# Performance work log

Measured on AMD Instinct MI355X. Metric: run time of the kernel, lower is better.

Reference implementation:

```python
import jax, jax.numpy as jnp
import numpy as np

N, E = 50000, 800000          # nodes, directed edges
IN_DIM, HC, OUT_DIM = 128, 64, 128
NEG_SLOPE = 0.2               # PyG GATConv default leaky_relu slope
EPS = 1e-5                    # PyG LayerNorm default eps


def setup_inputs() -> dict:
    key = jax.random.key(0)
    ks = jax.random.split(key, 10)
    s = 0.1
    return {
        "x": jax.random.normal(ks[0], (N, IN_DIM), jnp.float32),
        "edge_index": jax.random.randint(ks[1], (2, E), 0, N, dtype=jnp.int32),
        # conv1: GATConv(IN_DIM -> HC, heads=2, concat=True)
        "W1": jax.random.normal(ks[2], (IN_DIM, 2 * HC), jnp.float32) * s,
        "att_src1": jax.random.normal(ks[3], (2, HC), jnp.float32) * s,
        "att_dst1": jax.random.normal(ks[4], (2, HC), jnp.float32) * s,
        "b1": jnp.zeros((2 * HC,), jnp.float32),
        "ln1_w": jnp.ones((2 * HC,), jnp.float32),
        "ln1_b": jnp.zeros((2 * HC,), jnp.float32),
        # conv2: GATConv(2*HC -> OUT_DIM, heads=1, concat=False)
        "W2": jax.random.normal(ks[5], (2 * HC, OUT_DIM), jnp.float32) * s,
        "att_src2": jax.random.normal(ks[6], (1, OUT_DIM), jnp.float32) * s,
        "att_dst2": jax.random.normal(ks[7], (1, OUT_DIM), jnp.float32) * s,
        "b2": jnp.zeros((OUT_DIM,), jnp.float32),
        "ln2_w": jnp.ones((OUT_DIM,), jnp.float32),
        "ln2_b": jnp.zeros((OUT_DIM,), jnp.float32),
    }


def gat_conv(x, src, dst, W, att_src, att_dst, bias, heads, C, concat):
    """PyG GATConv (shared lin for src/dst, self-loops already in src/dst)."""
    n = x.shape[0]
    h = (x @ W).reshape(n, heads, C)                       # [N,H,C]
    a_src = jnp.einsum('nhc,hc->nh', h, att_src)           # [N,H]
    a_dst = jnp.einsum('nhc,hc->nh', h, att_dst)           # [N,H]
    e = jax.nn.leaky_relu(a_src[src] + a_dst[dst], NEG_SLOPE)   # [E',H]
    # numerically-stable softmax over incoming edges of each dst node
    emax = jax.ops.segment_max(e, dst, num_segments=n)     # [N,H] (self-loops => non-empty)
    ex = jnp.exp(e - emax[dst])
    denom = jax.ops.segment_sum(ex, dst, num_segments=n)
    alpha = ex / (denom[dst] + 1e-16)                      # [E',H]
    out = jax.ops.segment_sum(h[src] * alpha[:, :, None], dst, num_segments=n)  # [N,H,C]
    out = out.reshape(n, heads * C) if concat else out.mean(axis=1)
    return out + bias


def graph_layernorm(x, w, b):
    """PyG LayerNorm, mode='graph', single graph: normalize over ALL nodes+features."""
    mean = x.mean()
    xc = x - mean
    var = (xc * xc).mean()
    return xc * jax.lax.rsqrt(var + EPS) * w + b


def reference(x, edge_index, W1, att_src1, att_dst1, b1, ln1_w, ln1_b,
              W2, att_src2, att_dst2, b2, ln2_w, ln2_b):
    n = x.shape[0]
    loop = jnp.arange(n, dtype=edge_index.dtype)
    src = jnp.concatenate([edge_index[0], loop])           # add self-loops for GAT convs
    dst = jnp.concatenate([edge_index[1], loop])

    h = gat_conv(x, src, dst, W1, att_src1, att_dst1, b1, heads=2, C=HC, concat=True)
    h = jax.nn.relu(graph_layernorm(h, ln1_w, ln1_b))
    h = gat_conv(h, src, dst, W2, att_src2, att_dst2, b2, heads=1, C=OUT_DIM, concat=False)
    h = graph_layernorm(h, ln2_w, ln2_b)

    # SimpleConv(aggr='mean') over the ORIGINAL edges (no self-loops), then residual
    s0, d0 = edge_index[0], edge_index[1]
    agg = jax.ops.segment_sum(h[s0], d0, num_segments=n)
    cnt = jax.ops.segment_sum(jnp.ones(s0.shape, h.dtype), d0, num_segments=n)
    mean_agg = agg / jnp.maximum(cnt, 1.0)[:, None]
    return jax.nn.relu(mean_agg + x)
```

## Files before the change

### kernel.cpp

```cpp
#include <hip/hip_runtime.h>
#include <hip/hip_bf16.h>
#include <cstdint>
#include <cstddef>

#define NN 50000
#define EE 800000
#define DD 128
#define NEG 0.2f
#define EPSL 1e-5f

#define NB   392
#define NBKT 196
#define HM   (NBKT * NB)

#define GROWS 64

typedef __hip_bfloat16 bf16;
typedef short short8 __attribute__((ext_vector_type(8)));
typedef float f32x4 __attribute__((ext_vector_type(4)));

__device__ inline float bflo(unsigned u) { return __uint_as_float(u << 16); }
__device__ inline float bfhi(unsigned u) { return __uint_as_float(u & 0xffff0000u); }

__device__ inline unsigned short f2bf(float f) {
    __bf16 h = (__bf16)f;
    return __builtin_bit_cast(unsigned short, h);
}

__device__ inline void store4(float* Out, size_t idx, float4 v) {
    *(float4*)&Out[idx] = v;
}
__device__ inline void store4(bf16* Out, size_t idx, float4 v) {
    union { bf16 b[4]; ushort4 u; } cv;
    cv.b[0] = (bf16)v.x; cv.b[1] = (bf16)v.y; cv.b[2] = (bf16)v.z; cv.b[3] = (bf16)v.w;
    *(ushort4*)&Out[idx] = cv.u;
}


__global__ __launch_bounds__(256) void pack_hist_kernel(const int* __restrict__ ei,
                                                        unsigned* __restrict__ keys,
                                                        int* __restrict__ histG) {
    __shared__ int lh[NBKT];
    int tid = threadIdx.x;
    for (int t = tid; t < NBKT; t += 256) lh[t] = 0;
    __syncthreads();
    int base = blockIdx.x * 2048;
    #pragma unroll
    for (int j = 0; j < 8; ++j) {
        int i = base + j * 256 + tid;
        if (i < EE) {
            unsigned s = (unsigned)ei[i];
            unsigned d = (unsigned)ei[EE + i];
            keys[i] = (d << 16) | s;
            atomicAdd(&lh[d >> 8], 1);
        }
    }
    __syncthreads();
    for (int t = tid; t < NBKT; t += 256) histG[t * NB + blockIdx.x] = lh[t];
}

__global__ __launch_bounds__(1024) void scan_hist_kernel(const int* __restrict__ histG,
                                                         int* __restrict__ offs,
                                                         int* __restrict__ bstart) {
    __shared__ int wsum[16];
    __shared__ int carry_s;
    int tid = threadIdx.x, lane = tid & 63, wv = tid >> 6;
    if (tid == 0) carry_s = 0;
    __syncthreads();
    for (int base = 0; base < HM; base += 4096) {
        int i4 = base + tid * 4;
        int4 v = make_int4(0, 0, 0, 0);
        if (i4 + 3 < HM) v = *(const int4*)&histG[i4];
        else {
            if (i4 + 0 < HM) v.x = histG[i4 + 0];
            if (i4 + 1 < HM) v.y = histG[i4 + 1];
            if (i4 + 2 < HM) v.z = histG[i4 + 2];
            if (i4 + 3 < HM) v.w = histG[i4 + 3];
        }
        int tsum = v.x + v.y + v.z + v.w;
        int x = tsum;
        for (int off = 1; off < 64; off <<= 1) {
            int t = __shfl_up(x, off);
            if (lane >= off) x += t;
        }
        if (lane == 63) wsum[wv] = x;
        __syncthreads();
        if (wv == 0) {
            int s = (lane < 16) ? wsum[lane] : 0;
            for (int off = 1; off < 16; off <<= 1) {
                int t = __shfl_up(s, off);
                if (lane >= off) s += t;
            }
            if (lane < 16) wsum[lane] = s;
        }
        __syncthreads();
        int waveoff = (wv == 0) ? 0 : wsum[wv - 1];
        int carry = carry_s;
        int o0 = carry + waveoff + x - tsum;
        int o1 = o0 + v.x, o2 = o1 + v.y, o3 = o2 + v.z;
        if (i4 + 3 < HM) *(int4*)&offs[i4] = make_int4(o0, o1, o2, o3);
        else {
            if (i4 + 0 < HM) offs[i4 + 0] = o0;
            if (i4 + 1 < HM) offs[i4 + 1] = o1;
            if (i4 + 2 < HM) offs[i4 + 2] = o2;
            if (i4 + 3 < HM) offs[i4 + 3] = o3;
        }
        if (i4 < HM && (i4 % NB) == 0) bstart[i4 / NB] = o0;
        __syncthreads();
        if (tid == 0) carry_s += wsum[15];
        __syncthreads();
    }
    if (tid == 0) bstart[NBKT] = carry_s;
}

__global__ __launch_bounds__(256) void scatter_pass1_kernel(const unsigned* __restrict__ keys,
                                                            const int* __restrict__ offs,
                                                            unsigned* __restrict__ tmp) {
    __shared__ int lofs[NBKT];
    int tid = threadIdx.x;
    for (int t = tid; t < NBKT; t += 256) lofs[t] = offs[t * NB + blockIdx.x];
    __syncthreads();
    int base = blockIdx.x * 2048;
    #pragma unroll
    for (int j = 0; j < 8; ++j) {
        int i = base + j * 256 + tid;
        if (i < EE) {
            unsigned key = keys[i];
            int pos = atomicAdd(&lofs[key >> 24], 1);
            tmp[pos] = key;
        }
    }
}

__global__ __launch_bounds__(256) void bucket_sort_kernel(const unsigned* __restrict__ tmp,
                                                          const int* __restrict__ bstart,
                                                          unsigned* __restrict__ col,
                                                          int* __restrict__ row_ptr) {
    __shared__ int cnt[256];
    __shared__ int cpos[256];
    __shared__ int wtot[4];
    int tid = threadIdx.x, lane = tid & 63, wv = tid >> 6;
    int s0 = bstart[blockIdx.x], s1 = bstart[blockIdx.x + 1];
    cnt[tid] = 0;
    __syncthreads();
    for (int i = s0 + tid; i < s1; i += 256)
        atomicAdd(&cnt[(tmp[i] >> 16) & 0xFF], 1);
    __syncthreads();
    int v = cnt[tid];
    int x = v;
    for (int off = 1; off < 64; off <<= 1) {
        int t = __shfl_up(x, off);
        if (lane >= off) x += t;
    }
    if (lane == 63) wtot[wv] = x;
    __syncthreads();
    int add = 0;
    for (int k = 0; k < wv; ++k) add += wtot[k];
    int start = s0 + add + x - v;
    cpos[tid] = start;
    int d = blockIdx.x * 256 + tid;
    if (d <= NN) row_ptr[d] = start;
    __syncthreads();
    for (int i = s0 + tid; i < s1; i += 256) {
        unsigned key = tmp[i];
        int pos = atomicAdd(&cpos[(key >> 16) & 0xFF], 1);
        col[pos] = key;
    }
}

template <int H, bool LN>
__global__ __launch_bounds__(512) void gemm_attn(const float* __restrict__ X,
                                                 const float* __restrict__ W,
                                                 const float* __restrict__ att_s,
                                                 const float* __restrict__ att_d,
                                                 const double* __restrict__ stats,
                                                 const float* __restrict__ lnw,
                                                 const float* __restrict__ lnb,
                                                 bf16* __restrict__ Hout,
                                                 float* __restrict__ a_src,
                                                 float* __restrict__ a_dst) {
    __shared__ __align__(16) char lds[(128 * 136 + 64 * 136) * 2 + 2048];
    unsigned short* Bt = (unsigned short*)lds;
    unsigned short* As = (unsigned short*)(lds + 128 * 136 * 2);
    float* Cs = (float*)lds;
    float* psum = (float*)(lds + (128 * 136 + 64 * 136) * 2);

    int tid = threadIdx.x;
    int c = tid & 127, h4 = tid >> 7;
    int row0 = blockIdx.x * GROWS;

    float mean = 0.f, inv = 1.f, wc = 1.f, bc = 0.f;
    if (LN) {
        const double M = (double)NN * DD;
        double mean_d = stats[0] / M;
        double var_d = stats[1] / M - mean_d * mean_d;
        mean = (float)mean_d;
        inv = rsqrtf((float)var_d + EPSL);
        wc = lnw[c]; bc = lnb[c];
    }

    #pragma unroll 4
    for (int i = 0; i < 16; ++i) {
        int k0 = (i * 4 + h4) * 2;
        float wa = W[(size_t)k0 * DD + c];
        float wb = W[(size_t)(k0 + 1) * DD + c];
        unsigned pk = (unsigned)f2bf(wa) | ((unsigned)f2bf(wb) << 16);
        *(unsigned*)&Bt[c * 136 + k0] = pk;
    }
    #pragma unroll 4
    for (int i = 0; i < 16; ++i) {
        int r = i * 4 + h4;
        int row = row0 + r;
        float v = (row < NN) ? X[(size_t)row * DD + c] : 0.f;
        if (LN) v = fmaxf((v - mean) * inv * wc + bc, 0.f);
        As[r * 136 + c] = f2bf(v);
    }
    __syncthreads();

    int lane = tid & 63, w = tid >> 6;
    int rg = w & 3, cg = w >> 2;
    int l15 = lane & 15, quad = lane >> 4;
    f32x4 acc[4];
    #pragma unroll
    for (int t = 0; t < 4; ++t) acc[t] = 0.f;
    const unsigned short* Arow = As + (rg * 16 + l15) * 136 + quad * 8;
    const unsigned short* Brow = Bt + l15 * 136 + quad * 8;
    #pragma unroll
    for (int ks = 0; ks < 4; ++ks) {
        short8 a = *(const short8*)(Arow + ks * 32);
        #pragma unroll
        for (int tt = 0; tt < 4; ++tt) {
            short8 b = *(const short8*)(Brow + (cg * 4 + tt) * 16 * 136 + ks * 32);
            acc[tt] = __builtin_amdgcn_mfma_f32_16x16x32_bf16(a, b, acc[tt], 0, 0, 0);
        }
    }
    __syncthreads();

    #pragma unroll
    for (int tt = 0; tt < 4; ++tt)
        #pragma unroll
        for (int r = 0; r < 4; ++r)
            Cs[(rg * 16 + quad * 4 + r) * 132 + (cg * 4 + tt) * 16 + l15] = acc[tt][r];

    float ds[4] = {0.f, 0.f, 0.f, 0.f}, dd[4] = {0.f, 0.f, 0.f, 0.f};
    #pragma unroll
    for (int tt = 0; tt < 4; ++tt) {
        int cc = (cg * 4 + tt) * 16 + l15;
        float as_ = att_s[cc], ad_ = att_d[cc];
        #pragma unroll
        for (int r = 0; r < 4; ++r) {
            ds[r] = fmaf(acc[tt][r], as_, ds[r]);
            dd[r] = fmaf(acc[tt][r], ad_, dd[r]);
        }
    }
    #pragma unroll
    for (int off = 1; off < 16; off <<= 1) {
        #pragma unroll
        for (int r = 0; r < 4; ++r) {
            ds[r] += __shfl_xor(ds[r], off);
            dd[r] += __shfl_xor(dd[r], off);
        }
    }
    if (l15 == 0) {
        #pragma unroll
        for (int r = 0; r < 4; ++r) {
            int rr = rg * 16 + quad * 4 + r;
            int row = row0 + rr;
            if (H == 2) {
                if (row < NN) {
                    a_src[row * 2 + cg] = ds[r];
                    a_dst[row * 2 + cg] = dd[r];
                }
            } else {
                psum[cg * 64 + rr] = ds[r];
                psum[128 + cg * 64 + rr] = dd[r];
            }
        }
    }
    __syncthreads();

    if (H == 1 && tid < 64) {
        int row = row0 + tid;
        if (row < NN) {
            a_src[row] = psum[tid] + psum[64 + tid];
            a_dst[row] = psum[128 + tid] + psum[192 + tid];
        }
    }

    unsigned short* Hp = (unsigned short*)Hout;
    #pragma unroll 4
    for (int i = 0; i < 16; ++i) {
        int r = i * 4 + h4;
        int row = row0 + r;
        if (row < NN) Hp[(size_t)row * DD + c] = f2bf(Cs[r * 132 + c]);
    }
}

template <int H, typename OT>
__global__ __launch_bounds__(256) void gat_agg(const int* __restrict__ row_ptr,
                                               const unsigned* __restrict__ col,
                                               const bf16* __restrict__ Hin,
                                               const float* __restrict__ a_src,
                                               const float* __restrict__ a_dst,
                                               const float* __restrict__ bias,
                                               OT* __restrict__ Out,
                                               float2* __restrict__ pstats) {
    int tid = threadIdx.x;
    int sl = tid & 31;
    int n = blockIdx.x * 8 + (tid >> 5);
    int c0 = sl * 4;
    const int head4 = (H == 2) ? (sl >> 4) : 0;

    int beg = row_ptr[n], end = row_ptr[n + 1];
    int deg = end - beg;

    float ad0 = a_dst[n * H + 0];
    float ad1 = (H == 2) ? a_dst[n * H + 1] : 0.f;
    const ushort* Hp = (const ushort*)Hin + c0;

    float acc[4] = {0.f, 0.f, 0.f, 0.f};
    float dl0 = 0.f, dl1 = 0.f;

    for (int base = 0; base < deg; base += 32) {
        int ecnt = min(32, deg - base);
        int sv = 0; float w0v = 0.f, w1v = 0.f;
        if (sl < ecnt) {
            sv = (int)(col[beg + base + sl] & 0xffffu);
            if (H == 2) {
                float2 av = *(const float2*)&a_src[sv * 2];
                float e0 = av.x + ad0; e0 = (e0 > 0.f) ? e0 : NEG * e0;
                float e1 = av.y + ad1; e1 = (e1 > 0.f) ? e1 : NEG * e1;
                w0v = __expf(e0); w1v = __expf(e1);
                dl0 += w0v; dl1 += w1v;
            } else {
                float e0 = a_src[sv] + ad0; e0 = (e0 > 0.f) ? e0 : NEG * e0;
                w0v = __expf(e0);
                dl0 += w0v;
            }
        }
        int j = 0;
        for (; j + 7 < ecnt; j += 8) {
            int s[8]; float ww[8];
            uint2 h[8];
            #pragma unroll
            for (int u = 0; u < 8; ++u) {
                s[u] = __shfl(sv, j + u, 32);
                if (H == 2) {
                    float a0 = __shfl(w0v, j + u, 32), b0 = __shfl(w1v, j + u, 32);
                    ww[u] = head4 ? b0 : a0;
                } else {
                    ww[u] = __shfl(w0v, j + u, 32);
                }
            }
            #pragma unroll
            for (int u = 0; u < 8; ++u) h[u] = *(const uint2*)(Hp + (size_t)s[u] * DD);
            #pragma unroll
            for (int u = 0; u < 8; ++u) {
                acc[0] = fmaf(ww[u], bflo(h[u].x), acc[0]);
                acc[1] = fmaf(ww[u], bfhi(h[u].x), acc[1]);
                acc[2] = fmaf(ww[u], bflo(h[u].y), acc[2]);
                acc[3] = fmaf(ww[u], bfhi(h[u].y), acc[3]);
            }
        }
        for (; j < ecnt; ++j) {
            int s = __shfl(sv, j, 32);
            float w;
            if (H == 2) {
                float a0 = __shfl(w0v, j, 32), b0 = __shfl(w1v, j, 32);
                w = head4 ? b0 : a0;
            } else {
                w = __shfl(w0v, j, 32);
            }
            uint2 hv = *(const uint2*)(Hp + (size_t)s * DD);
            acc[0] = fmaf(w, bflo(hv.x), acc[0]); acc[1] = fmaf(w, bfhi(hv.x), acc[1]);
            acc[2] = fmaf(w, bflo(hv.y), acc[2]); acc[3] = fmaf(w, bfhi(hv.y), acc[3]);
        }
    }

    #pragma unroll
    for (int off = 1; off < 32; off <<= 1) {
        dl0 += __shfl_xor(dl0, off);
        if (H == 2) dl1 += __shfl_xor(dl1, off);
    }

    float e0 = a_src[n * H + 0] + ad0; e0 = (e0 > 0.f) ? e0 : NEG * e0;
    float ws0 = __expf(e0);
    float ws1 = 0.f;
    if (H == 2) {
        float e1 = a_src[n * H + 1] + ad1; e1 = (e1 > 0.f) ? e1 : NEG * e1;
        ws1 = __expf(e1);
    }
    float den = (H == 2 && head4) ? (dl1 + ws1) : (dl0 + ws0);
    float wself = (H == 2 && head4) ? ws1 : ws0;
    float rinv = 1.f / (den + 1e-16f);
    uint2 hs = *(const uint2*)(Hp + (size_t)n * DD);
    float4 bi = *(const float4*)&bias[c0];
    float4 o;
    o.x = fmaf(wself, bflo(hs.x), acc[0]) * rinv + bi.x;
    o.y = fmaf(wself, bfhi(hs.x), acc[1]) * rinv + bi.y;
    o.z = fmaf(wself, bflo(hs.y), acc[2]) * rinv + bi.z;
    o.w = fmaf(wself, bfhi(hs.y), acc[3]) * rinv + bi.w;
    store4(Out, (size_t)n * DD + c0, o);

    float t1 = o.x + o.y + o.z + o.w;
    float t2 = o.x * o.x + o.y * o.y + o.z * o.z + o.w * o.w;
    #pragma unroll
    for (int off = 1; off < 32; off <<= 1) {
        t1 += __shfl_xor(t1, off);
        t2 += __shfl_xor(t2, off);
    }
    if (sl == 0) pstats[n] = make_float2(t1, t2);
}

__global__ __launch_bounds__(1024) void reduce_stats_kernel(const float2* __restrict__ pstats,
                                                            double* __restrict__ stats) {
    int tid = threadIdx.x, lane = tid & 63, wv = tid >> 6;
    double s1 = 0.0, s2 = 0.0;
    for (int i = tid; i < NN; i += 1024) {
        float2 v = pstats[i];
        s1 += (double)v.x; s2 += (double)v.y;
    }
    for (int off = 32; off; off >>= 1) {
        s1 += __shfl_xor(s1, off);
        s2 += __shfl_xor(s2, off);
    }
    __shared__ double w1[16], w2[16];
    if (lane == 0) { w1[wv] = s1; w2[wv] = s2; }
    __syncthreads();
    if (tid == 0) {
        double a = 0.0, b = 0.0;
        for (int i = 0; i < 16; ++i) { a += w1[i]; b += w2[i]; }
        stats[0] = a; stats[1] = b;
    }
}

__global__ __launch_bounds__(256) void simpleconv_kernel(const int* __restrict__ row_ptr,
                                                         const unsigned* __restrict__ col,
                                                         const bf16* __restrict__ Hin,
                                                         const float* __restrict__ X,
                                                         const double* __restrict__ stats,
                                                         const float* __restrict__ lnw,
                                                         const float* __restrict__ lnb,
                                                         float* __restrict__ Out) {
    int tid = threadIdx.x;
    int sl = tid & 31;
    int n = blockIdx.x * 8 + (tid >> 5);
    int c0 = sl * 4;
    int beg = row_ptr[n], end = row_ptr[n + 1];
    int deg = end - beg;
    const ushort* Hp = (const ushort*)Hin + c0;

    float acc[4] = {0.f, 0.f, 0.f, 0.f};
    for (int base = 0; base < deg; base += 32) {
        int ecnt = min(32, deg - base);
        int sv = 0;
        if (sl < ecnt) sv = (int)(col[beg + base + sl] & 0xffffu);
        int j = 0;
        for (; j + 7 < ecnt; j += 8) {
            int s[8]; uint2 h[8];
            #pragma unroll
            for (int u = 0; u < 8; ++u) s[u] = __shfl(sv, j + u, 32);
            #pragma unroll
            for (int u = 0; u < 8; ++u) h[u] = *(const uint2*)(Hp + (size_t)s[u] * DD);
            #pragma unroll
            for (int u = 0; u < 8; ++u) {
                acc[0] += bflo(h[u].x); acc[1] += bfhi(h[u].x);
                acc[2] += bflo(h[u].y); acc[3] += bfhi(h[u].y);
            }
        }
        for (; j < ecnt; ++j) {
            int s = __shfl(sv, j, 32);
            uint2 hv = *(const uint2*)(Hp + (size_t)s * DD);
            acc[0] += bflo(hv.x); acc[1] += bfhi(hv.x);
            acc[2] += bflo(hv.y); acc[3] += bfhi(hv.y);
        }
    }

    const double M = (double)NN * DD;
    double mean_d = stats[0] / M;
    double var_d = stats[1] / M - mean_d * mean_d;
    float mean2 = (float)mean_d;
    float inv2 = rsqrtf((float)var_d + EPSL);
    float rc = 1.f / (float)((deg > 0) ? deg : 1);
    float4 xr = *(const float4*)&X[(size_t)n * DD + c0];
    float4 o;
    if (deg > 0) {
        float4 lw = *(const float4*)&lnw[c0];
        float4 lb = *(const float4*)&lnb[c0];
        o.x = (acc[0] * rc - mean2) * inv2 * lw.x + lb.x;
        o.y = (acc[1] * rc - mean2) * inv2 * lw.y + lb.y;
        o.z = (acc[2] * rc - mean2) * inv2 * lw.z + lb.z;
        o.w = (acc[3] * rc - mean2) * inv2 * lw.w + lb.w;
    } else {
        o.x = o.y = o.z = o.w = 0.f;
    }
    o.x = fmaxf(o.x + xr.x, 0.f);
    o.y = fmaxf(o.y + xr.y, 0.f);
    o.z = fmaxf(o.z + xr.z, 0.f);
    o.w = fmaxf(o.w + xr.w, 0.f);
    *(float4*)&Out[(size_t)n * DD + c0] = o;
}

extern "C" void kernel_launch(void* const* d_in, const int* in_sizes, int n_in,
                              void* d_out, int out_size, void* d_ws, size_t ws_size,
                              hipStream_t stream) {
    const float* x    = (const float*)d_in[0];
    const int*   ei   = (const int*)d_in[1];
    const float* W1   = (const float*)d_in[2];
    const float* as1  = (const float*)d_in[3];
    const float* ad1  = (const float*)d_in[4];
    const float* b1   = (const float*)d_in[5];
    const float* ln1w = (const float*)d_in[6];
    const float* ln1b = (const float*)d_in[7];
    const float* W2   = (const float*)d_in[8];
    const float* as2  = (const float*)d_in[9];
    const float* ad2  = (const float*)d_in[10];
    const float* b2   = (const float*)d_in[11];
    const float* ln2w = (const float*)d_in[12];
    const float* ln2b = (const float*)d_in[13];
    float* out = (float*)d_out;

    char* p = (char*)d_ws;
    auto alloc = [&](size_t bytes) {
        void* r = (void*)p;
        p += (bytes + 255) & ~(size_t)255;
        return r;
    };
    unsigned* keys    = (unsigned*)alloc((size_t)EE * 4);
    unsigned* tmp     = (unsigned*)alloc((size_t)EE * 4);
    unsigned* col     = (unsigned*)alloc((size_t)EE * 4);
    int*      histG   = (int*)alloc((size_t)HM * 4);
    int*      offs    = (int*)alloc((size_t)HM * 4);
    int*      bstart  = (int*)alloc((size_t)(NBKT + 1) * 4);
    int*      row_ptr = (int*)alloc((size_t)(NN + 256) * 4);
    double*   stats1  = (double*)alloc(16);
    double*   stats2  = (double*)alloc(16);
    float2*   pstats  = (float2*)alloc((size_t)NN * 8);
    bf16*     bufH    = (bf16*)alloc((size_t)NN * DD * 2);
    float*    bufF    = (float*)alloc((size_t)NN * DD * 4);
    bf16*     out2    = (bf16*)bufF;
    float*    aS1     = (float*)alloc((size_t)NN * 2 * 4);
    float*    aD1     = (float*)alloc((size_t)NN * 2 * 4);
    float*    aS2     = (float*)alloc((size_t)NN * 4);
    float*    aD2     = (float*)alloc((size_t)NN * 4);

    pack_hist_kernel<<<NB, 256, 0, stream>>>(ei, keys, histG);
    scan_hist_kernel<<<1, 1024, 0, stream>>>(histG, offs, bstart);
    scatter_pass1_kernel<<<NB, 256, 0, stream>>>(keys, offs, tmp);
    bucket_sort_kernel<<<NBKT, 256, 0, stream>>>(tmp, bstart, col, row_ptr);

    const int GB = (NN + GROWS - 1) / GROWS;
    const int AB = NN / 8;

    gemm_attn<2, false><<<GB, 512, 0, stream>>>(x, W1, as1, ad1,
                                                nullptr, nullptr, nullptr,
                                                bufH, aS1, aD1);
    gat_agg<2, float><<<AB, 256, 0, stream>>>(row_ptr, col, bufH, aS1, aD1, b1, bufF, pstats);
    reduce_stats_kernel<<<1, 1024, 0, stream>>>(pstats, stats1);

    gemm_attn<1, true><<<GB, 512, 0, stream>>>(bufF, W2, as2, ad2,
                                               stats1, ln1w, ln1b,
                                               bufH, aS2, aD2);
    gat_agg<1, bf16><<<AB, 256, 0, stream>>>(row_ptr, col, bufH, aS2, aD2, b2, out2, pstats);
    reduce_stats_kernel<<<1, 1024, 0, stream>>>(pstats, stats2);

    simpleconv_kernel<<<AB, 256, 0, stream>>>(row_ptr, col, out2, x,
                                              stats2, ln2w, ln2b, out);
}
```

Before: 321.3 us.

## Drop keys buffer, halve sort blocks, and vectorize GEMM staging loads/stores

The histogram kernel no longer writes a packed keys array; the scatter pass rebuilds each key directly from edge_index. This removes one 3.2 MB write and read in exchange for a second read of the source row. The sort block count is halved to 196 with 4096 edges per block, which shrinks the histogram scan. Separately, gemm_attn now stages W four k-values at a time and X as float4, and writes H as ushort4, to cut the number of memory instructions.

```diff
diff --git a/kernel.cpp b/kernel.cpp
--- a/kernel.cpp
+++ b/kernel.cpp
@@ -9,7 +9,8 @@
 #define NEG 0.2f
 #define EPSL 1e-5f
 
-#define NB   392
+#define NB   196
+#define EPB  4096
 #define NBKT 196
 #define HM   (NBKT * NB)
 
@@ -25,6 +26,9 @@
 __device__ inline unsigned short f2bf(float f) {
     __bf16 h = (__bf16)f;
     return __builtin_bit_cast(unsigned short, h);
+}
+__device__ inline unsigned pack2(float a, float b) {
+    return (unsigned)f2bf(a) | ((unsigned)f2bf(b) << 16);
 }
 
 __device__ inline void store4(float* Out, size_t idx, float4 v) {
@@ -37,21 +41,18 @@
 }
 
 
-__global__ __launch_bounds__(256) void pack_hist_kernel(const int* __restrict__ ei,
-                                                        unsigned* __restrict__ keys,
-                                                        int* __restrict__ histG) {
+__global__ __launch_bounds__(256) void hist_kernel(const int* __restrict__ ei,
+                                                   int* __restrict__ histG) {
     __shared__ int lh[NBKT];
     int tid = threadIdx.x;
     for (int t = tid; t < NBKT; t += 256) lh[t] = 0;
     __syncthreads();
-    int base = blockIdx.x * 2048;
-    #pragma unroll
-    for (int j = 0; j < 8; ++j) {
+    int base = blockIdx.x * EPB;
+    #pragma unroll
+    for (int j = 0; j < EPB / 256; ++j) {
         int i = base + j * 256 + tid;
         if (i < EE) {
-            unsigned s = (unsigned)ei[i];
             unsigned d = (unsigned)ei[EE + i];
-            keys[i] = (d << 16) | s;
             atomicAdd(&lh[d >> 8], 1);
         }
     }
@@ -113,20 +114,22 @@
     if (tid == 0) bstart[NBKT] = carry_s;
 }
 
-__global__ __launch_bounds__(256) void scatter_pass1_kernel(const unsigned* __restrict__ keys,
+__global__ __launch_bounds__(256) void scatter_pass1_kernel(const int* __restrict__ ei,
                                                             const int* __restrict__ offs,
                                                             unsigned* __restrict__ tmp) {
     __shared__ int lofs[NBKT];
     int tid = threadIdx.x;
     for (int t = tid; t < NBKT; t += 256) lofs[t] = offs[t * NB + blockIdx.x];
     __syncthreads();
-    int base = blockIdx.x * 2048;
-    #pragma unroll
-    for (int j = 0; j < 8; ++j) {
+    int base = blockIdx.x * EPB;
+    #pragma unroll
+    for (int j = 0; j < EPB / 256; ++j) {
         int i = base + j * 256 + tid;
         if (i < EE) {
-            unsigned key = keys[i];
-            int pos = atomicAdd(&lofs[key >> 24], 1);
+            unsigned s = (unsigned)ei[i];
+            unsigned d = (unsigned)ei[EE + i];
+            unsigned key = (d << 16) | s;
+            int pos = atomicAdd(&lofs[d >> 8], 1);
             tmp[pos] = key;
         }
     }
@@ -186,34 +189,50 @@
     float* psum = (float*)(lds + (128 * 136 + 64 * 136) * 2);
 
     int tid = threadIdx.x;
-    int c = tid & 127, h4 = tid >> 7;
     int row0 = blockIdx.x * GROWS;
 
-    float mean = 0.f, inv = 1.f, wc = 1.f, bc = 0.f;
-    if (LN) {
-        const double M = (double)NN * DD;
-        double mean_d = stats[0] / M;
-        double var_d = stats[1] / M - mean_d * mean_d;
-        mean = (float)mean_d;
-        inv = rsqrtf((float)var_d + EPSL);
-        wc = lnw[c]; bc = lnb[c];
-    }
-
-    #pragma unroll 4
-    for (int i = 0; i < 16; ++i) {
-        int k0 = (i * 4 + h4) * 2;
-        float wa = W[(size_t)k0 * DD + c];
-        float wb = W[(size_t)(k0 + 1) * DD + c];
-        unsigned pk = (unsigned)f2bf(wa) | ((unsigned)f2bf(wb) << 16);
-        *(unsigned*)&Bt[c * 136 + k0] = pk;
-    }
-    #pragma unroll 4
-    for (int i = 0; i < 16; ++i) {
-        int r = i * 4 + h4;
-        int row = row0 + r;
-        float v = (row < NN) ? X[(size_t)row * DD + c] : 0.f;
-        if (LN) v = fmaxf((v - mean) * inv * wc + bc, 0.f);
-        As[r * 136 + c] = f2bf(v);
+    {
+        int c = tid & 127, kg = tid >> 7;
+        #pragma unroll 2
+        for (int i = 0; i < 8; ++i) {
+            int k0 = i * 16 + kg * 4;
+            float wa = W[(size_t)(k0 + 0) * DD + c];
+            float wb = W[(size_t)(k0 + 1) * DD + c];
+            float wcv = W[(size_t)(k0 + 2) * DD + c];
+            float wdv = W[(size_t)(k0 + 3) * DD + c];
+            uint2 pk = make_uint2(pack2(wa, wb), pack2(wcv, wdv));
+            *(uint2*)&Bt[c * 136 + k0] = pk;
+        }
+    }
+    {
+        int sub = tid & 31, rq = tid >> 5;
+        int c4 = sub * 4;
+        float mean = 0.f, inv = 1.f;
+        float4 lw4 = make_float4(1.f, 1.f, 1.f, 1.f), lb4 = make_float4(0.f, 0.f, 0.f, 0.f);
+        if (LN) {
+            const double M = (double)NN * DD;
+            double mean_d = stats[0] / M;
+            double var_d = stats[1] / M - mean_d * mean_d;
+            mean = (float)mean_d;
+            inv = rsqrtf((float)var_d + EPSL);
+            lw4 = *(const float4*)&lnw[c4];
+            lb4 = *(const float4*)&lnb[c4];
+        }
+        #pragma unroll
+        for (int i = 0; i < 4; ++i) {
+            int r = i * 16 + rq;
+            int row = row0 + r;
+            float4 xv = make_float4(0.f, 0.f, 0.f, 0.f);
+            if (row < NN) xv = *(const float4*)&X[(size_t)row * DD + c4];
+            if (LN) {
+                xv.x = fmaxf((xv.x - mean) * inv * lw4.x + lb4.x, 0.f);
+                xv.y = fmaxf((xv.y - mean) * inv * lw4.y + lb4.y, 0.f);
+                xv.z = fmaxf((xv.z - mean) * inv * lw4.z + lb4.z, 0.f);
+                xv.w = fmaxf((xv.w - mean) * inv * lw4.w + lb4.w, 0.f);
+            }
+            uint2 pk = make_uint2(pack2(xv.x, xv.y), pack2(xv.z, xv.w));
+            *(uint2*)&As[r * 136 + c4] = pk;
+        }
     }
     __syncthreads();
 
@@ -287,12 +306,22 @@
         }
     }
 
-    unsigned short* Hp = (unsigned short*)Hout;
-    #pragma unroll 4
-    for (int i = 0; i < 16; ++i) {
-        int r = i * 4 + h4;
-        int row = row0 + r;
-        if (row < NN) Hp[(size_t)row * DD + c] = f2bf(Cs[r * 132 + c]);
+    {
+        int sub = tid & 31, rq = tid >> 5;
+        int c4 = sub * 4;
+        unsigned short* Hp = (unsigned short*)Hout;
+        #pragma unroll
+        for (int i = 0; i < 4; ++i) {
+            int r = i * 16 + rq;
+            int row = row0 + r;
+            if (row < NN) {
+                float4 cv = *(const float4*)&Cs[r * 132 + c4];
+                ushort4 pk;
+                pk.x = f2bf(cv.x); pk.y = f2bf(cv.y);
+                pk.z = f2bf(cv.z); pk.w = f2bf(cv.w);
+                *(ushort4*)&Hp[(size_t)row * DD + c4] = pk;
+            }
+        }
     }
 }
 
@@ -526,7 +555,6 @@
         p += (bytes + 255) & ~(size_t)255;
         return r;
     };
-    unsigned* keys    = (unsigned*)alloc((size_t)EE * 4);
     unsigned* tmp     = (unsigned*)alloc((size_t)EE * 4);
     unsigned* col     = (unsigned*)alloc((size_t)EE * 4);
     int*      histG   = (int*)alloc((size_t)HM * 4);
@@ -544,9 +572,9 @@
     float*    aS2     = (float*)alloc((size_t)NN * 4);
     float*    aD2     = (float*)alloc((size_t)NN * 4);
 
-    pack_hist_kernel<<<NB, 256, 0, stream>>>(ei, keys, histG);
+    hist_kernel<<<NB, 256, 0, stream>>>(ei, histG);
     scan_hist_kernel<<<1, 1024, 0, stream>>>(histG, offs, bstart);
-    scatter_pass1_kernel<<<NB, 256, 0, stream>>>(keys, offs, tmp);
+    scatter_pass1_kernel<<<NB, 256, 0, stream>>>(ei, offs, tmp);
     bucket_sort_kernel<<<NBKT, 256, 0, stream>>>(tmp, bstart, col, row_ptr);
 
     const int GB = (NN + GROWS - 1) / GROWS;
```

After: 296.1 us. 1.09x faster.
